# Kernel tuning notes

Measured on AMD Instinct MI355X. Metric: run time of the kernel, lower is better.

Reference implementation:

```python
import jax, jax.numpy as jnp
import numpy as np

K = 3       # kernel_size
STRIDE = 1


def setup_inputs() -> dict:
    key = jax.random.key(0)
    k1, k2, k3 = jax.random.split(key, 3)
    B, C, H, W = 128, 64, 32, 32
    O = 64
    OH = (H - K) // STRIDE + 1  # 30
    OW = (W - K) // STRIDE + 1  # 30
    x = jax.random.normal(k1, (B, C, H, W), dtype=jnp.float32)
    weight = jax.random.normal(k2, (O, C, OH, OW, K, K), dtype=jnp.float32)
    bias = jax.random.normal(k3, (O, OH, OW), dtype=jnp.float32)
    return {"x": x, "weight": weight, "bias": bias}


def reference(x, weight, bias):
    # x: [B, C, H, W]; weight: [O, C, OH, OW, K, K]; bias: [O, OH, OW]
    O, C, OH, OW, _, _ = weight.shape
    # Extract all k x k patches in one pass: [B, C*K*K, OH, OW],
    # feature axis ordered (C, kh, kw) with spatial fastest.
    patches = jax.lax.conv_general_dilated_patches(
        x, filter_shape=(K, K), window_strides=(STRIDE, STRIDE), padding="VALID"
    )
    # Faithful to torch einsum 'bcih,coih->bo': the region's channel axis is
    # contracted against the weight's FIRST axis (nominal out_channels), and the
    # output channel is the weight's SECOND axis (requires C == O).
    # Rearrange weight -> [C*K*K (contract), O (output), OH, OW].
    w = jnp.transpose(weight, (0, 4, 5, 1, 2, 3)).reshape(C * K * K, O, OH, OW)
    out = jnp.einsum("bpij,poij->boij", patches, w) + bias[None]
    return out  # [B, O, OH, OW]
```

## Files before the change

### kernel.cpp

```cpp
#include <hip/hip_runtime.h>


#define BDIM 256

typedef __bf16 bf16x4 __attribute__((ext_vector_type(4)));
typedef __bf16 bf16x8 __attribute__((ext_vector_type(8)));
typedef float f32x4 __attribute__((ext_vector_type(4)));

__device__ __forceinline__ unsigned short f2bf(float f) {
  union { float f; unsigned u; } v; v.f = f;
  unsigned r = v.u + 0x7fffu + ((v.u >> 16) & 1u);
  return (unsigned short)(r >> 16);
}
__device__ __forceinline__ unsigned long long pk3(unsigned short a, unsigned short b,
                                                  unsigned short c) {
  return (unsigned long long)a | ((unsigned long long)b << 16) | ((unsigned long long)c << 32);
}


__global__ __launch_bounds__(256, 2) void lcl_kernel(
    const float* __restrict__ x, const float* __restrict__ wgt,
    const float* __restrict__ bias, float* __restrict__ out) {
  int blk = blockIdx.x;
  int xcd = blk & 7, sg = blk >> 3;
  int t = xcd * 56 + (xcd < 2 ? xcd : 2) + sg;
  int i  = t / 15;
  int j0 = (t % 15) * 2;
  int ij0 = i * 30 + j0;

  __shared__ __align__(16) unsigned short Aslab[128 * 196];
  __shared__ __align__(16) unsigned short Bt[2 * 64 * 104];

  const int tid  = threadIdx.x;
  const int wave = tid >> 6;
  const int lane = tid & 63;
  const int lrow = lane & 15;
  const int q    = lane >> 4;

  f32x4 acc[2][2][4];
#pragma unroll
  for (int a = 0; a < 2; ++a)
#pragma unroll
    for (int b = 0; b < 2; ++b)
#pragma unroll
      for (int c = 0; c < 4; ++c) acc[a][b][c] = f32x4{0.f, 0.f, 0.f, 0.f};

  float2 av[12][2];
  float2 wv[2][9];

#define LOAD_CHUNK(C0)                                                          \
  {                                                                             \
    const int c0_ = (C0);                                                       \
    _Pragma("unroll")                                                           \
    for (int k = 0; k < 12; ++k) {                                              \
      int r  = tid + k * 256;                                                   \
      int kh = r % 3;                                                           \
      int cc = (r / 3) & 7;                                                     \
      int b  = r / 24;                                                          \
      const float2* xp = (const float2*)(x + b * 65536 + (c0_ + cc) * 1024 +    \
                                         (i + kh) * 32 + j0);                   \
      av[k][0] = xp[0];                                                         \
      av[k][1] = xp[1];                                                         \
    }                                                                           \
    _Pragma("unroll")                                                           \
    for (int p = 0; p < 2; ++p) {                                               \
      int pr = tid + p * 256;                                                   \
      int o = pr & 63, cc = pr >> 6;                                            \
      const float2* wp = (const float2*)(wgt + (c0_ + cc) * 518400 + o * 8100 + \
                                         ij0 * 9);                              \
      _Pragma("unroll")                                                         \
      for (int e = 0; e < 9; ++e) wv[p][e] = wp[e];                             \
    }                                                                           \
  }

  LOAD_CHUNK(0)

  for (int chunk = 0; chunk < 8; ++chunk) {
    if (chunk) __syncthreads();

#pragma unroll
    for (int k = 0; k < 12; ++k) {
      int r  = tid + k * 256;
      int kh = r % 3;
      int cc = (r / 3) & 7;
      int b  = r / 24;
      int g  = cc * 3 + kh;
      unsigned short h0 = f2bf(av[k][0].x), h1 = f2bf(av[k][0].y);
      unsigned short h2 = f2bf(av[k][1].x), h3 = f2bf(av[k][1].y);
      *(unsigned long long*)&Aslab[b * 196 + g * 8]     = pk3(h0, h1, h2);
      *(unsigned long long*)&Aslab[b * 196 + g * 8 + 4] = pk3(h1, h2, h3);
    }
#pragma unroll
    for (int p = 0; p < 2; ++p) {
      int pr = tid + p * 256;
      int o = pr & 63, cc = pr >> 6;
#pragma unroll
      for (int jj = 0; jj < 2; ++jj)
#pragma unroll
        for (int kh = 0; kh < 3; ++kh) {
          int e0 = jj * 9 + kh * 3;
          float f0 = (e0 & 1) ? wv[p][e0 >> 1].y : wv[p][e0 >> 1].x;
          float f1 = ((e0 + 1) & 1) ? wv[p][(e0 + 1) >> 1].y : wv[p][(e0 + 1) >> 1].x;
          float f2v = ((e0 + 2) & 1) ? wv[p][(e0 + 2) >> 1].y : wv[p][(e0 + 2) >> 1].x;
          *(unsigned long long*)&Bt[jj * 6656 + o * 104 + (cc * 3 + kh) * 4] =
              pk3(f2bf(f0), f2bf(f1), f2bf(f2v));
        }
    }
    __syncthreads();

    if (chunk < 7) LOAD_CHUNK((chunk + 1) * 8)

#pragma unroll
    for (int s = 0; s < 3; ++s) {
      bf16x8 bfr[2][4];
#pragma unroll
      for (int jj = 0; jj < 2; ++jj)
#pragma unroll
        for (int nt = 0; nt < 4; ++nt)
          bfr[jj][nt] = *reinterpret_cast<const bf16x8*>(
              &Bt[jj * 6656 + (nt * 16 + lrow) * 104 + s * 32 + q * 8]);
#pragma unroll
      for (int mt = 0; mt < 2; ++mt) {
        int b  = wave * 32 + mt * 16 + lrow;
        int ga = s * 8 + q * 2;
#pragma unroll
        for (int jj = 0; jj < 2; ++jj) {
          bf16x4 lo = *reinterpret_cast<const bf16x4*>(&Aslab[b * 196 + (ga * 2 + jj) * 4]);
          bf16x4 hi = *reinterpret_cast<const bf16x4*>(&Aslab[b * 196 + (ga * 2 + 2 + jj) * 4]);
          bf16x8 af = __builtin_shufflevector(lo, hi, 0, 1, 2, 3, 4, 5, 6, 7);
#pragma unroll
          for (int nt = 0; nt < 4; ++nt)
            acc[mt][jj][nt] = __builtin_amdgcn_mfma_f32_16x16x32_bf16(
                af, bfr[jj][nt], acc[mt][jj][nt], 0, 0, 0);
        }
      }
    }
  }

#pragma unroll
  for (int nt = 0; nt < 4; ++nt) {
    int o = nt * 16 + lrow;
    float2 bv = *(const float2*)(bias + o * 900 + ij0);
#pragma unroll
    for (int mt = 0; mt < 2; ++mt) {
#pragma unroll
      for (int r = 0; r < 4; ++r) {
        int b = wave * 32 + mt * 16 + q * 4 + r;
        float2 res;
        res.x = acc[mt][0][nt][r] + bv.x;
        res.y = acc[mt][1][nt][r] + bv.y;
        *(float2*)(out + b * 57600 + o * 900 + ij0) = res;
      }
    }
  }
}

extern "C" void kernel_launch(void* const* d_in, const int* in_sizes, int n_in,
                              void* d_out, int out_size, void* d_ws, size_t ws_size,
                              hipStream_t stream) {
  const float* x    = (const float*)d_in[0];
  const float* wgt  = (const float*)d_in[1];
  const float* bias = (const float*)d_in[2];
  float* out        = (float*)d_out;
  lcl_kernel<<<dim3(450), dim3(256), 0, stream>>>(x, wgt, bias, out);
}
```

Baseline: 318.3 us.

## Split batch across two blocks, keep im2col A fragments in registers, double-buffer weights

Launches 900 blocks instead of 450, with each block handling half the batch (64 rows) for one output pixel pair. The input patch fragments now go straight from global loads into MFMA operand registers, so the shared-memory A slab and its stores are gone. The weight tile in LDS is double-buffered, which removes one barrier per chunk, and the weight load mapping is remapped so lanes read contiguous spans. Occupancy hint is raised to 3 blocks per CU. The trade-off is that each weight tile is now loaded by two blocks, doubling weight traffic per output, and the per-element scattered short stores into LDS may cause bank conflicts.

```diff
diff --git a/kernel.cpp b/kernel.cpp
--- a/kernel.cpp
+++ b/kernel.cpp
@@ -3,33 +3,36 @@
 
 #define BDIM 256
 
-typedef __bf16 bf16x4 __attribute__((ext_vector_type(4)));
 typedef __bf16 bf16x8 __attribute__((ext_vector_type(8)));
 typedef float f32x4 __attribute__((ext_vector_type(4)));
+typedef unsigned long long u64;
 
 __device__ __forceinline__ unsigned short f2bf(float f) {
   union { float f; unsigned u; } v; v.f = f;
   unsigned r = v.u + 0x7fffu + ((v.u >> 16) & 1u);
   return (unsigned short)(r >> 16);
 }
-__device__ __forceinline__ unsigned long long pk3(unsigned short a, unsigned short b,
-                                                  unsigned short c) {
-  return (unsigned long long)a | ((unsigned long long)b << 16) | ((unsigned long long)c << 32);
+
+__device__ __forceinline__ bf16x8 mk_af(u64 lo, u64 hi) {
+  union { u64 q[2]; bf16x8 v; } u;
+  u.q[0] = lo; u.q[1] = hi;
+  return u.v;
 }
 
 
-__global__ __launch_bounds__(256, 2) void lcl_kernel(
+__global__ __launch_bounds__(256, 3) void lcl_kernel(
     const float* __restrict__ x, const float* __restrict__ wgt,
     const float* __restrict__ bias, float* __restrict__ out) {
-  int blk = blockIdx.x;
-  int xcd = blk & 7, sg = blk >> 3;
-  int t = xcd * 56 + (xcd < 2 ? xcd : 2) + sg;
-  int i  = t / 15;
-  int j0 = (t % 15) * 2;
+  int bid = blockIdx.x;
+  int xcd = bid & 7, sg = bid >> 3;
+  int wg = (xcd < 4 ? xcd * 113 : 452 + (xcd - 4) * 112) + sg;
+  int t    = wg >> 1;
+  int half = wg & 1;
+  int i   = t / 15;
+  int j0  = (t % 15) * 2;
   int ij0 = i * 30 + j0;
 
-  __shared__ __align__(16) unsigned short Aslab[128 * 196];
-  __shared__ __align__(16) unsigned short Bt[2 * 64 * 104];
+  __shared__ __align__(16) unsigned short Bt[2 * 2 * 64 * 104];
 
   const int tid  = threadIdx.x;
   const int wave = tid >> 6;
@@ -37,78 +40,95 @@
   const int lrow = lane & 15;
   const int q    = lane >> 4;
 
-  f32x4 acc[2][2][4];
+  {
+    u64* zp = (u64*)Bt;
+#pragma unroll
+    for (int k = 0; k < 26; ++k) zp[tid + k * 256] = 0ull;
+  }
+
+  const int b_x = half * 64 + wave * 16 + lrow;
+  const float* xp[3][2];
+#pragma unroll
+  for (int s = 0; s < 3; ++s)
+#pragma unroll
+    for (int tt = 0; tt < 2; ++tt) {
+      int g  = s * 8 + q * 2 + tt;
+      int cc = g / 3, kh = g % 3;
+      xp[s][tt] = x + b_x * 65536 + cc * 1024 + (i + kh) * 32 + j0;
+    }
+
+  int p9 = lane / 9;
+  int e9 = lane - p9 * 9;
+  int U  = wave * 7 + p9;
+  const char* wbase = (const char*)wgt + (size_t)U * 32400 +
+                      (size_t)(ij0 * 9 + e9 * 2) * 4;
+  int f0 = 2 * e9, f1 = f0 + 1;
+  int r0 = f0 % 9, r1 = f1 % 9;
+  int sl0 = (f0 / 9) * 6656 + (r0 / 3) * 4 + (r0 % 3);
+  int sl1 = (f1 / 9) * 6656 + (r1 / 3) * 4 + (r1 % 3);
+
+  float2 av[3][2][2];
+  float2 wv[19];
+
+#define LOAD_X(C0)                                                        \
+  _Pragma("unroll") for (int s = 0; s < 3; ++s)                           \
+  _Pragma("unroll") for (int tt = 0; tt < 2; ++tt) {                      \
+    const float2* xq = (const float2*)(xp[s][tt] + (C0) * 1024);          \
+    av[s][tt][0] = xq[0];                                                 \
+    av[s][tt][1] = xq[1];                                                 \
+  }
+
+#define LOAD_W(C0)                                                        \
+  {                                                                       \
+    const char* wb = wbase + (size_t)(C0) * 2073600;                      \
+    _Pragma("unroll") for (int ps = 0; ps < 18; ++ps)                     \
+      wv[ps] = *(const float2*)(wb + ps * 907200);                        \
+    if (U < 8) wv[18] = *(const float2*)(wb + 18 * 907200);               \
+    else       wv[18] = float2{0.f, 0.f};                                 \
+  }
+
+  f32x4 acc[2][4];
 #pragma unroll
   for (int a = 0; a < 2; ++a)
 #pragma unroll
-    for (int b = 0; b < 2; ++b)
-#pragma unroll
-      for (int c = 0; c < 4; ++c) acc[a][b][c] = f32x4{0.f, 0.f, 0.f, 0.f};
+    for (int n = 0; n < 4; ++n) acc[a][n] = f32x4{0.f, 0.f, 0.f, 0.f};
 
-  float2 av[12][2];
-  float2 wv[2][9];
-
-#define LOAD_CHUNK(C0)                                                          \
-  {                                                                             \
-    const int c0_ = (C0);                                                       \
-    _Pragma("unroll")                                                           \
-    for (int k = 0; k < 12; ++k) {                                              \
-      int r  = tid + k * 256;                                                   \
-      int kh = r % 3;                                                           \
-      int cc = (r / 3) & 7;                                                     \
-      int b  = r / 24;                                                          \
-      const float2* xp = (const float2*)(x + b * 65536 + (c0_ + cc) * 1024 +    \
-                                         (i + kh) * 32 + j0);                   \
-      av[k][0] = xp[0];                                                         \
-      av[k][1] = xp[1];                                                         \
-    }                                                                           \
-    _Pragma("unroll")                                                           \
-    for (int p = 0; p < 2; ++p) {                                               \
-      int pr = tid + p * 256;                                                   \
-      int o = pr & 63, cc = pr >> 6;                                            \
-      const float2* wp = (const float2*)(wgt + (c0_ + cc) * 518400 + o * 8100 + \
-                                         ij0 * 9);                              \
-      _Pragma("unroll")                                                         \
-      for (int e = 0; e < 9; ++e) wv[p][e] = wp[e];                             \
-    }                                                                           \
-  }
-
-  LOAD_CHUNK(0)
+  LOAD_X(0)
+  LOAD_W(0)
 
   for (int chunk = 0; chunk < 8; ++chunk) {
-    if (chunk) __syncthreads();
+    unsigned short* B = Bt + (chunk & 1) * 13312;
 
 #pragma unroll
-    for (int k = 0; k < 12; ++k) {
-      int r  = tid + k * 256;
-      int kh = r % 3;
-      int cc = (r / 3) & 7;
-      int b  = r / 24;
-      int g  = cc * 3 + kh;
-      unsigned short h0 = f2bf(av[k][0].x), h1 = f2bf(av[k][0].y);
-      unsigned short h2 = f2bf(av[k][1].x), h3 = f2bf(av[k][1].y);
-      *(unsigned long long*)&Aslab[b * 196 + g * 8]     = pk3(h0, h1, h2);
-      *(unsigned long long*)&Aslab[b * 196 + g * 8 + 4] = pk3(h1, h2, h3);
+    for (int ps = 0; ps < 19; ++ps) {
+      if (ps < 18 || U < 8) {
+        int P  = ps * 28 + U;
+        int cc = P >> 6, o = P & 63;
+        int sb = cc * 12 + o * 104;
+        B[sb + sl0] = f2bf(wv[ps].x);
+        B[sb + sl1] = f2bf(wv[ps].y);
+      }
     }
+
+    u64 rb[3][2];
 #pragma unroll
-    for (int p = 0; p < 2; ++p) {
-      int pr = tid + p * 256;
-      int o = pr & 63, cc = pr >> 6;
+    for (int s = 0; s < 3; ++s)
 #pragma unroll
-      for (int jj = 0; jj < 2; ++jj)
-#pragma unroll
-        for (int kh = 0; kh < 3; ++kh) {
-          int e0 = jj * 9 + kh * 3;
-          float f0 = (e0 & 1) ? wv[p][e0 >> 1].y : wv[p][e0 >> 1].x;
-          float f1 = ((e0 + 1) & 1) ? wv[p][(e0 + 1) >> 1].y : wv[p][(e0 + 1) >> 1].x;
-          float f2v = ((e0 + 2) & 1) ? wv[p][(e0 + 2) >> 1].y : wv[p][(e0 + 2) >> 1].x;
-          *(unsigned long long*)&Bt[jj * 6656 + o * 104 + (cc * 3 + kh) * 4] =
-              pk3(f2bf(f0), f2bf(f1), f2bf(f2v));
-        }
-    }
+      for (int tt = 0; tt < 2; ++tt) {
+        unsigned short h0 = f2bf(av[s][tt][0].x);
+        unsigned short h1 = f2bf(av[s][tt][0].y);
+        unsigned short h2 = f2bf(av[s][tt][1].x);
+        unsigned short h3 = f2bf(av[s][tt][1].y);
+        rb[s][tt] = (u64)h0 | ((u64)h1 << 16) | ((u64)h2 << 32) |
+                    ((u64)h3 << 48);
+      }
+
     __syncthreads();
 
-    if (chunk < 7) LOAD_CHUNK((chunk + 1) * 8)
+    if (chunk < 7) {
+      LOAD_X((chunk + 1) * 8)
+      LOAD_W((chunk + 1) * 8)
+    }
 
 #pragma unroll
     for (int s = 0; s < 3; ++s) {
@@ -118,49 +138,42 @@
 #pragma unroll
         for (int nt = 0; nt < 4; ++nt)
           bfr[jj][nt] = *reinterpret_cast<const bf16x8*>(
-              &Bt[jj * 6656 + (nt * 16 + lrow) * 104 + s * 32 + q * 8]);
+              &B[jj * 6656 + (nt * 16 + lrow) * 104 + s * 32 + q * 8]);
 #pragma unroll
-      for (int mt = 0; mt < 2; ++mt) {
-        int b  = wave * 32 + mt * 16 + lrow;
-        int ga = s * 8 + q * 2;
+      for (int jj = 0; jj < 2; ++jj) {
+        u64 lo = (rb[s][0] >> (jj * 16)) & 0x0000FFFFFFFFFFFFull;
+        u64 hi = (rb[s][1] >> (jj * 16)) & 0x0000FFFFFFFFFFFFull;
+        bf16x8 af = mk_af(lo, hi);
 #pragma unroll
-        for (int jj = 0; jj < 2; ++jj) {
-          bf16x4 lo = *reinterpret_cast<const bf16x4*>(&Aslab[b * 196 + (ga * 2 + jj) * 4]);
-          bf16x4 hi = *reinterpret_cast<const bf16x4*>(&Aslab[b * 196 + (ga * 2 + 2 + jj) * 4]);
-          bf16x8 af = __builtin_shufflevector(lo, hi, 0, 1, 2, 3, 4, 5, 6, 7);
-#pragma unroll
-          for (int nt = 0; nt < 4; ++nt)
-            acc[mt][jj][nt] = __builtin_amdgcn_mfma_f32_16x16x32_bf16(
-                af, bfr[jj][nt], acc[mt][jj][nt], 0, 0, 0);
-        }
+        for (int nt = 0; nt < 4; ++nt)
+          acc[jj][nt] = __builtin_amdgcn_mfma_f32_16x16x32_bf16(
+              af, bfr[jj][nt], acc[jj][nt], 0, 0, 0);
       }
     }
   }
 
+  const int b_out = half * 64 + wave * 16 + q * 4;
 #pragma unroll
   for (int nt = 0; nt < 4; ++nt) {
     int o = nt * 16 + lrow;
     float2 bv = *(const float2*)(bias + o * 900 + ij0);
 #pragma unroll
-    for (int mt = 0; mt < 2; ++mt) {
-#pragma unroll
-      for (int r = 0; r < 4; ++r) {
-        int b = wave * 32 + mt * 16 + q * 4 + r;
-        float2 res;
-        res.x = acc[mt][0][nt][r] + bv.x;
-        res.y = acc[mt][1][nt][r] + bv.y;
-        *(float2*)(out + b * 57600 + o * 900 + ij0) = res;
-      }
+    for (int r = 0; r < 4; ++r) {
+      int b = b_out + r;
+      float2 res;
+      res.x = acc[0][nt][r] + bv.x;
+      res.y = acc[1][nt][r] + bv.y;
+      *(float2*)(out + b * 57600 + o * 900 + ij0) = res;
     }
   }
 }
 
 extern "C" void kernel_launch(void* const* d_in, const int* in_sizes, int n_in,
-                              void* d_out, int out_size, void* d_ws, size_t ws_size,
-                              hipStream_t stream) {
+                              void* d_out, int out_size, void* d_ws,
+                              size_t ws_size, hipStream_t stream) {
   const float* x    = (const float*)d_in[0];
   const float* wgt  = (const float*)d_in[1];
   const float* bias = (const float*)d_in[2];
   float* out        = (float*)d_out;
-  lcl_kernel<<<dim3(450), dim3(256), 0, stream>>>(x, wgt, bias, out);
+  lcl_kernel<<<dim3(900), dim3(256), 0, stream>>>(x, wgt, bias, out);
 }
```

Measured after the change: 338.8 us. 6.4% more time.

## Load A fragments directly into registers, drop A LDS slab, double-buffer B

Applied to the files above, without the earlier changes.

Each lane now loads its own x patch rows as float4 directly from global memory and builds the bf16 A operand in registers with shifts, eliminating the A shared-memory slab and its store/load round trip. The B weight tile is double-buffered in LDS, which removes one barrier per chunk, and the weights are loaded as wider float4 vectors with a changed bf16 packing layout. Padding slots are zeroed once up front. The cost is more global load requests per lane, including some redundancy across lanes, and higher register pressure.

```diff
diff --git a/kernel.cpp b/kernel.cpp
--- a/kernel.cpp
+++ b/kernel.cpp
@@ -1,20 +1,26 @@
 #include <hip/hip_runtime.h>
 
 
-#define BDIM 256
-
-typedef __bf16 bf16x4 __attribute__((ext_vector_type(4)));
 typedef __bf16 bf16x8 __attribute__((ext_vector_type(8)));
 typedef float f32x4 __attribute__((ext_vector_type(4)));
+typedef unsigned long long u64;
+typedef unsigned int u32t;
+typedef unsigned short u16t;
 
-__device__ __forceinline__ unsigned short f2bf(float f) {
-  union { float f; unsigned u; } v; v.f = f;
-  unsigned r = v.u + 0x7fffu + ((v.u >> 16) & 1u);
-  return (unsigned short)(r >> 16);
+struct __attribute__((packed, aligned(8))) uf4 { f32x4 v; };
+
+__device__ __forceinline__ u16t f2bf(float f) {
+  union { float f; u32t u; } v; v.f = f;
+  u32t r = v.u + 0x7fffu + ((v.u >> 16) & 1u);
+  return (u16t)(r >> 16);
 }
-__device__ __forceinline__ unsigned long long pk3(unsigned short a, unsigned short b,
-                                                  unsigned short c) {
-  return (unsigned long long)a | ((unsigned long long)b << 16) | ((unsigned long long)c << 32);
+__device__ __forceinline__ u32t pk2(float a, float b) {
+  return (u32t)f2bf(a) | ((u32t)f2bf(b) << 16);
+}
+__device__ __forceinline__ bf16x8 mk_af(u64 lo, u64 hi) {
+  union { u64 q[2]; bf16x8 v; } u;
+  u.q[0] = lo; u.q[1] = hi;
+  return u.v;
 }
 
 
@@ -24,18 +30,60 @@
   int blk = blockIdx.x;
   int xcd = blk & 7, sg = blk >> 3;
   int t = xcd * 56 + (xcd < 2 ? xcd : 2) + sg;
-  int i  = t / 15;
+  int i = t / 15;
   int j0 = (t % 15) * 2;
   int ij0 = i * 30 + j0;
 
-  __shared__ __align__(16) unsigned short Aslab[128 * 196];
-  __shared__ __align__(16) unsigned short Bt[2 * 64 * 104];
+  __shared__ __align__(16) u16t Bt[2 * 2 * 64 * 104];
 
   const int tid  = threadIdx.x;
   const int wave = tid >> 6;
   const int lane = tid & 63;
   const int lrow = lane & 15;
   const int q    = lane >> 4;
+
+  {
+    u64* zp = (u64*)Bt;
+#pragma unroll
+    for (int k = 0; k < 26; ++k) zp[tid + k * 256] = 0ull;
+  }
+
+  int xoffF[3][2];
+#pragma unroll
+  for (int s = 0; s < 3; ++s)
+#pragma unroll
+    for (int tt = 0; tt < 2; ++tt) {
+      int g = s * 8 + q * 2 + tt, cc = g / 3, kh = g - cc * 3;
+      xoffF[s][tt] = cc * 1024 + kh * 32;
+    }
+  const float* xb0 = x + (wave * 32 + lrow) * 65536 + i * 32 + j0;
+  const float* xb1 = xb0 + 16 * 65536;
+
+  const int o_w = tid & 63;
+  const float* wb0 = wgt + (size_t)wave * 518400 + o_w * 8100 + ij0 * 9;
+  const float* wb1 = wb0 + (size_t)4 * 518400;
+
+  f32x4 av[2][3][2];
+  f32x4 wv[2][5];
+
+#define LOAD_CHUNK(C0)                                                        \
+  {                                                                           \
+    const float* xc0 = xb0 + (C0) * 1024;                                     \
+    const float* xc1 = xb1 + (C0) * 1024;                                     \
+    _Pragma("unroll") for (int s = 0; s < 3; ++s)                             \
+    _Pragma("unroll") for (int tt = 0; tt < 2; ++tt) {                        \
+      av[0][s][tt] = ((const uf4*)(xc0 + xoffF[s][tt]))->v;                   \
+      av[1][s][tt] = ((const uf4*)(xc1 + xoffF[s][tt]))->v;                   \
+    }                                                                         \
+    const float* w0 = wb0 + (size_t)(C0) * 518400;                            \
+    const float* w1 = wb1 + (size_t)(C0) * 518400;                            \
+    _Pragma("unroll") for (int e = 0; e < 4; ++e) {                           \
+      wv[0][e] = ((const uf4*)(w0 + e * 4))->v;                               \
+      wv[1][e] = ((const uf4*)(w1 + e * 4))->v;                               \
+    }                                                                         \
+    wv[0][4] = ((const uf4*)(w0 + 14))->v;                                    \
+    wv[1][4] = ((const uf4*)(w1 + 14))->v;                                    \
+  }
 
   f32x4 acc[2][2][4];
 #pragma unroll
@@ -45,67 +93,44 @@
 #pragma unroll
       for (int c = 0; c < 4; ++c) acc[a][b][c] = f32x4{0.f, 0.f, 0.f, 0.f};
 
-  float2 av[12][2];
-  float2 wv[2][9];
-
-#define LOAD_CHUNK(C0)                                                          \
-  {                                                                             \
-    const int c0_ = (C0);                                                       \
-    _Pragma("unroll")                                                           \
-    for (int k = 0; k < 12; ++k) {                                              \
-      int r  = tid + k * 256;                                                   \
-      int kh = r % 3;                                                           \
-      int cc = (r / 3) & 7;                                                     \
-      int b  = r / 24;                                                          \
-      const float2* xp = (const float2*)(x + b * 65536 + (c0_ + cc) * 1024 +    \
-                                         (i + kh) * 32 + j0);                   \
-      av[k][0] = xp[0];                                                         \
-      av[k][1] = xp[1];                                                         \
-    }                                                                           \
-    _Pragma("unroll")                                                           \
-    for (int p = 0; p < 2; ++p) {                                               \
-      int pr = tid + p * 256;                                                   \
-      int o = pr & 63, cc = pr >> 6;                                            \
-      const float2* wp = (const float2*)(wgt + (c0_ + cc) * 518400 + o * 8100 + \
-                                         ij0 * 9);                              \
-      _Pragma("unroll")                                                         \
-      for (int e = 0; e < 9; ++e) wv[p][e] = wp[e];                             \
-    }                                                                           \
-  }
-
   LOAD_CHUNK(0)
 
   for (int chunk = 0; chunk < 8; ++chunk) {
-    if (chunk) __syncthreads();
+    u16t* B = Bt + (chunk & 1) * 13312;
 
 #pragma unroll
-    for (int k = 0; k < 12; ++k) {
-      int r  = tid + k * 256;
-      int kh = r % 3;
-      int cc = (r / 3) & 7;
-      int b  = r / 24;
-      int g  = cc * 3 + kh;
-      unsigned short h0 = f2bf(av[k][0].x), h1 = f2bf(av[k][0].y);
-      unsigned short h2 = f2bf(av[k][1].x), h3 = f2bf(av[k][1].y);
-      *(unsigned long long*)&Aslab[b * 196 + g * 8]     = pk3(h0, h1, h2);
-      *(unsigned long long*)&Aslab[b * 196 + g * 8 + 4] = pk3(h1, h2, h3);
+    for (int p = 0; p < 2; ++p) {
+      int ccl = wave + 4 * p;
+      u16t* Bp = B + o_w * 104 + ccl * 12;
+      *(u32t*)&Bp[0] = pk2(wv[p][0][0], wv[p][0][1]);
+      Bp[2]  = f2bf(wv[p][0][2]);
+      Bp[4]  = f2bf(wv[p][0][3]);
+      Bp[5]  = f2bf(wv[p][1][0]);
+      Bp[6]  = f2bf(wv[p][1][1]);
+      *(u32t*)&Bp[8] = pk2(wv[p][1][2], wv[p][1][3]);
+      Bp[10] = f2bf(wv[p][2][0]);
+      u16t* Bq = Bp + 6656;
+      *(u32t*)&Bq[0] = pk2(wv[p][2][1], wv[p][2][2]);
+      Bq[2]  = f2bf(wv[p][2][3]);
+      Bq[4]  = f2bf(wv[p][3][0]);
+      Bq[5]  = f2bf(wv[p][3][1]);
+      Bq[6]  = f2bf(wv[p][3][2]);
+      *(u32t*)&Bq[8] = pk2(wv[p][3][3], wv[p][4][2]);
+      Bq[10] = f2bf(wv[p][4][3]);
     }
+
+    u64 rb[2][3][2];
 #pragma unroll
-    for (int p = 0; p < 2; ++p) {
-      int pr = tid + p * 256;
-      int o = pr & 63, cc = pr >> 6;
+    for (int mt = 0; mt < 2; ++mt)
 #pragma unroll
-      for (int jj = 0; jj < 2; ++jj)
+      for (int s = 0; s < 3; ++s)
 #pragma unroll
-        for (int kh = 0; kh < 3; ++kh) {
-          int e0 = jj * 9 + kh * 3;
-          float f0 = (e0 & 1) ? wv[p][e0 >> 1].y : wv[p][e0 >> 1].x;
-          float f1 = ((e0 + 1) & 1) ? wv[p][(e0 + 1) >> 1].y : wv[p][(e0 + 1) >> 1].x;
-          float f2v = ((e0 + 2) & 1) ? wv[p][(e0 + 2) >> 1].y : wv[p][(e0 + 2) >> 1].x;
-          *(unsigned long long*)&Bt[jj * 6656 + o * 104 + (cc * 3 + kh) * 4] =
-              pk3(f2bf(f0), f2bf(f1), f2bf(f2v));
+        for (int tt = 0; tt < 2; ++tt) {
+          const f32x4 vv = av[mt][s][tt];
+          rb[mt][s][tt] =
+              (u64)pk2(vv[0], vv[1]) | ((u64)pk2(vv[2], vv[3]) << 32);
         }
-    }
+
     __syncthreads();
 
     if (chunk < 7) LOAD_CHUNK((chunk + 1) * 8)
@@ -118,22 +143,19 @@
 #pragma unroll
         for (int nt = 0; nt < 4; ++nt)
           bfr[jj][nt] = *reinterpret_cast<const bf16x8*>(
-              &Bt[jj * 6656 + (nt * 16 + lrow) * 104 + s * 32 + q * 8]);
+              &B[jj * 6656 + (nt * 16 + lrow) * 104 + s * 32 + q * 8]);
 #pragma unroll
-      for (int mt = 0; mt < 2; ++mt) {
-        int b  = wave * 32 + mt * 16 + lrow;
-        int ga = s * 8 + q * 2;
+      for (int mt = 0; mt < 2; ++mt)
 #pragma unroll
         for (int jj = 0; jj < 2; ++jj) {
-          bf16x4 lo = *reinterpret_cast<const bf16x4*>(&Aslab[b * 196 + (ga * 2 + jj) * 4]);
-          bf16x4 hi = *reinterpret_cast<const bf16x4*>(&Aslab[b * 196 + (ga * 2 + 2 + jj) * 4]);
-          bf16x8 af = __builtin_shufflevector(lo, hi, 0, 1, 2, 3, 4, 5, 6, 7);
+          u64 lo = rb[mt][s][0] >> (jj * 16);
+          u64 hi = rb[mt][s][1] >> (jj * 16);
+          bf16x8 af = mk_af(lo, hi);
 #pragma unroll
           for (int nt = 0; nt < 4; ++nt)
             acc[mt][jj][nt] = __builtin_amdgcn_mfma_f32_16x16x32_bf16(
                 af, bfr[jj][nt], acc[mt][jj][nt], 0, 0, 0);
         }
-      }
     }
   }
 
@@ -156,8 +178,8 @@
 }
 
 extern "C" void kernel_launch(void* const* d_in, const int* in_sizes, int n_in,
-                              void* d_out, int out_size, void* d_ws, size_t ws_size,
-                              hipStream_t stream) {
+                              void* d_out, int out_size, void* d_ws,
+                              size_t ws_size, hipStream_t stream) {
   const float* x    = (const float*)d_in[0];
   const float* wgt  = (const float*)d_in[1];
   const float* bias = (const float*)d_in[2];
```

Measured after the change: 314.1 us. About the same (-1.3%).
